# Kernel optimization log

Hardware: AMD Instinct MI355X
Metric: run time of the kernel (lower is better)

Reference implementation:

```python
import jax, jax.numpy as jnp
import numpy as np

HEADS = 16
LN_EPS = 1e-5


def setup_inputs() -> dict:
    key = jax.random.key(0)
    ks = jax.random.split(key, 12)
    B, IMG, Q, H = 8192, 2048, 768, 1024
    def init(k, shape, fan_in):
        return jax.random.normal(k, shape, dtype=jnp.float32) * (fan_in ** -0.5)
    return {
        "features1": jax.random.normal(ks[0], (B, IMG), dtype=jnp.float32),
        "features2": jax.random.normal(ks[1], (B, Q), dtype=jnp.float32),
        "W1": init(ks[2], (IMG, H), IMG),
        "b1": jnp.zeros((H,), dtype=jnp.float32),
        "W2": init(ks[3], (Q, H), Q),
        "b2": jnp.zeros((H,), dtype=jnp.float32),
        "Wqkv": init(ks[4], (H, 3 * H), H),
        "Wout": init(ks[5], (H, H), H),
        "bout": jnp.zeros((H,), dtype=jnp.float32),
        "gamma": jnp.ones((2 * H,), dtype=jnp.float32),
        "beta": jnp.zeros((2 * H,), dtype=jnp.float32),
    }


def reference(features1, features2, W1, b1, W2, b2, Wqkv, Wout, bout, gamma, beta):
    B = features1.shape[0]
    H = W1.shape[1]
    hd = H // HEADS
    scale = hd ** -0.5
    # modality projections -> [B, H] each
    f1 = features1 @ W1 + b1
    f2 = features2 @ W2 + b2
    x = jnp.stack([f1, f2], axis=1)                      # [B, 2, H]
    qkv = x @ Wqkv                                       # [B, 2, 3H]
    q, k, v = jnp.split(qkv, 3, axis=-1)
    # b n (h d) -> b h n d
    def to_heads(t):
        return t.reshape(B, 2, HEADS, hd).transpose(0, 2, 1, 3)
    q, k, v = to_heads(q) * scale, to_heads(k), to_heads(v)
    attn = jnp.einsum('bhid,bhjd->bhij', q, k)           # [B, h, 2, 2]
    attn = jax.nn.softmax(attn, axis=-1)
    out = jnp.einsum('bhij,bhjd->bhid', attn, v)         # [B, h, 2, d]
    out = out.transpose(0, 2, 1, 3).reshape(B, 2, H)     # b h n d -> b n (h d)
    out = out @ Wout + bout                              # [B, 2, H]
    flat = out.reshape(B, 2 * H)
    # LayerNorm over last dim
    mu = jnp.mean(flat, axis=-1, keepdims=True)
    var = jnp.var(flat, axis=-1, keepdims=True)
    normed = (flat - mu) * jax.lax.rsqrt(var + LN_EPS) * gamma + beta
    # dropout in eval mode = identity
    res = jnp.concatenate([f1, f2], axis=1)              # [B, 2H]
    return normed + res
```

## Files before the change

kernel.cpp:

```cpp
#include <hip/hip_runtime.h>
#include <hip/hip_bf16.h>
#include <cstdint>

typedef __attribute__((ext_vector_type(8))) short short8;
typedef __attribute__((ext_vector_type(4))) short short4v;
typedef __attribute__((ext_vector_type(4))) float floatx4;
typedef __attribute__((ext_vector_type(4))) unsigned short ushort4v;

__device__ __forceinline__ float bf2f(unsigned short u) {
    union { unsigned int u; float f; } v;
    v.u = ((unsigned int)u) << 16;
    return v.f;
}
__device__ __forceinline__ unsigned short f2bf(float f) {
    union { float f; unsigned int u; } v; v.f = f;
    unsigned int u = v.u;
    unsigned int r = (u + 0x7FFFu + ((u >> 16) & 1u)) >> 16;
    return (unsigned short)r;
}
__device__ __forceinline__ float lo_bf(unsigned int u) {
    union { unsigned int u; float f; } v; v.u = u << 16; return v.f;
}
__device__ __forceinline__ float hi_bf(unsigned int u) {
    union { unsigned int u; float f; } v; v.u = u & 0xffff0000u; return v.f;
}
__device__ __forceinline__ void gld_lds16(const void* g, void* l) {
    __builtin_amdgcn_global_load_lds(
        (const __attribute__((address_space(1))) unsigned int*)g,
        (__attribute__((address_space(3))) unsigned int*)l,
        16, 0, 0);
}

__global__ __launch_bounds__(256) void prep_kernel(
    const float* __restrict__ f1, const float* __restrict__ f2,
    unsigned short* __restrict__ f1b, unsigned short* __restrict__ f2b,
    const float* __restrict__ W1, unsigned short* __restrict__ W1t,
    const float* __restrict__ W2, unsigned short* __restrict__ W2t,
    const float* __restrict__ Wqkv, unsigned short* __restrict__ Wqkvt,
    const float* __restrict__ Wout, unsigned short* __restrict__ Woutt) {
    __shared__ float tile[64][33];
    const int b = blockIdx.x;
    const int tid = threadIdx.x;

    if (b < 5632) {
        const float* in = (b < 4096) ? f1 : f2;
        unsigned short* outp = (b < 4096) ? f1b : f2b;
        int base = ((b < 4096) ? b : (b - 4096)) * 1024 + tid;
#pragma unroll
        for (int it = 0; it < 4; it++) {
            int i = base + it * 256;
            float4 v = ((const float4*)in)[i];
            ushort4v o;
            o.x = f2bf(v.x); o.y = f2bf(v.y); o.z = f2bf(v.z); o.w = f2bf(v.w);
            ((ushort4v*)outp)[i] = o;
        }
        return;
    }

    const float* in; unsigned short* outp; int K, N, t;
    if (b < 6656)      { in = W1;   outp = W1t;   K = 2048; N = 1024; t = b - 5632; }
    else if (b < 7040) { in = W2;   outp = W2t;   K = 768;  N = 1024; t = b - 6656; }
    else if (b < 8576) { in = Wqkv; outp = Wqkvt; K = 1024; N = 3072; t = b - 7040; }
    else               { in = Wout; outp = Woutt; K = 1024; N = 1024; t = b - 8576; }
    const int ntiles = N >> 5;
    const int n0 = (t % ntiles) * 32;
    const int k0 = (t / ntiles) * 64;
    const int tx = tid & 31, tg = tid >> 5;
#pragma unroll
    for (int i = 0; i < 8; i++)
        tile[tg * 8 + i][tx] = in[(size_t)(k0 + tg * 8 + i) * N + n0 + tx];
    __syncthreads();
    const int n = tid >> 3, kc = (tid & 7) * 8;
    short8 o;
#pragma unroll
    for (int j = 0; j < 8; j++) o[j] = (short)f2bf(tile[kc + j][n]);
    *(short8*)&outp[(size_t)(n0 + n) * K + k0 + kc] = o;
}

template <bool OUT_BF16, bool HAS_BIAS>
__device__ __forceinline__ void gemm_core(const unsigned short* __restrict__ A,
                                          const unsigned short* __restrict__ Bt,
                                          void* __restrict__ Cv, const float* __restrict__ bias,
                                          int K, int ldc, int blockM, int blockN,
                                          unsigned short* As, unsigned short* Bs) {
    const int tid  = threadIdx.x;
    const int lane = tid & 63;
    const int wave = tid >> 6;
    const int wm = wave >> 1, wn = wave & 1;

    const int kx = (tid >> 3) & 3;
    const unsigned short* gA = A  + (size_t)(blockM + (tid >> 2)) * K + ((tid & 3) ^ kx) * 8;
    const unsigned short* gB = Bt + (size_t)(blockN + (tid >> 2)) * K + ((tid & 3) ^ kx) * 8;
    const size_t sK = (size_t)64 * K;
    unsigned short* lA = As + wave * 512;
    unsigned short* lB = Bs + wave * 512;

    floatx4 acc[4][4];
#pragma unroll
    for (int i = 0; i < 4; i++)
#pragma unroll
        for (int j = 0; j < 4; j++) acc[i][j] = (floatx4){0.f, 0.f, 0.f, 0.f};

    const int col  = lane & 15;
    const int quad = lane >> 4;
    const int qx = quad ^ ((col >> 1) & 3);
    const int aoff32 = (wm * 64 + col) * 32 + qx * 8;
    const int boff32 = (wn * 64 + col) * 32 + qx * 8;

    const int kIters = K >> 6;
    for (int kt = 0; kt < kIters; ++kt) {
        const size_t ko = (size_t)kt * 64;
        gld_lds16(gA + ko,           lA);
        gld_lds16(gA + sK + ko,      lA + 2048);
        gld_lds16(gA + 32 + ko,      lA + 4096);
        gld_lds16(gA + sK + 32 + ko, lA + 6144);
        gld_lds16(gB + ko,           lB);
        gld_lds16(gB + sK + ko,      lB + 2048);
        gld_lds16(gB + 32 + ko,      lB + 4096);
        gld_lds16(gB + sK + 32 + ko, lB + 6144);
        __syncthreads();

#pragma unroll
        for (int hh = 0; hh < 2; hh++) {
            short8 a[4];
#pragma unroll
            for (int i = 0; i < 4; i++) a[i] = *(const short8*)&As[hh * 4096 + aoff32 + i * 512];
#pragma unroll
            for (int j = 0; j < 4; j++) {
                short8 bj = *(const short8*)&Bs[hh * 4096 + boff32 + j * 512];
#pragma unroll
                for (int i = 0; i < 4; i++)
                    acc[i][j] = __builtin_amdgcn_mfma_f32_16x16x32_bf16(a[i], bj, acc[i][j], 0, 0, 0);
            }
        }
        __syncthreads();
    }

#pragma unroll
    for (int i = 0; i < 4; i++) {
#pragma unroll
        for (int j = 0; j < 4; j++) {
#pragma unroll
            for (int r = 0; r < 4; r++) {
                int row = blockM + wm * 64 + i * 16 + quad * 4 + r;
                int cn  = blockN + wn * 64 + j * 16 + col;
                float v = acc[i][j][r];
                if (HAS_BIAS) v += bias[cn];
                if (OUT_BF16) ((unsigned short*)Cv)[(size_t)row * ldc + cn] = f2bf(v);
                else          ((float*)Cv)[(size_t)row * ldc + cn] = v;
            }
        }
    }
}

__global__ __launch_bounds__(256, 3)
void gemm_f12(const unsigned short* __restrict__ f1b, const unsigned short* __restrict__ W1t,
              const float* __restrict__ b1,
              const unsigned short* __restrict__ f2b, const unsigned short* __restrict__ W2t,
              const float* __restrict__ b2, unsigned short* __restrict__ xb) {
    __shared__ alignas(16) unsigned short As[8192];
    __shared__ alignas(16) unsigned short Bs[8192];
    const int blockM = blockIdx.x * 128;
    const int blockN = blockIdx.y * 128;
    if (blockIdx.z == 0)
        gemm_core<true, true>(f1b, W1t, (void*)xb, b1, 2048, 2048, blockM, blockN, As, Bs);
    else
        gemm_core<true, true>(f2b, W2t, (void*)(xb + 1024), b2, 768, 2048, blockM, blockN, As, Bs);
}

__global__ __launch_bounds__(256, 3)
void gemm_proj(const unsigned short* __restrict__ attn, const unsigned short* __restrict__ Woutt,
               const float* __restrict__ bout, unsigned short* __restrict__ projb) {
    __shared__ alignas(16) unsigned short As[8192];
    __shared__ alignas(16) unsigned short Bs[8192];
    gemm_core<true, true>(attn, Woutt, (void*)projb, bout, 1024, 1024,
                          blockIdx.x * 128, blockIdx.y * 128, As, Bs);
}

#define T2_STRIDE 132
__global__ __launch_bounds__(256, 3)
void gemm_qkv_attn(const unsigned short* __restrict__ A, const unsigned short* __restrict__ Bt,
                   unsigned short* __restrict__ attn_out) {
    __shared__ alignas(16) char smem[52224];
    unsigned short* As = (unsigned short*)smem;
    unsigned short* Bs = As + 8192;
    unsigned short* T2 = (unsigned short*)smem;
    float* wsm = (float*)(smem + 50688);

    const int tid  = threadIdx.x;
    const int lane = tid & 63;
    const int wave = tid >> 6;
    const int g = blockIdx.x;
    const int h = g >> 7;
    const int blockM = (g & 127) * 128;
    const int wm = wave >> 1, wn = wave & 1;
    const int K = 1024;

    const int kx = (tid >> 3) & 3;
    const unsigned short* gA = A  + (size_t)(blockM + (tid >> 2)) * K + ((tid & 3) ^ kx) * 8;
    const unsigned short* gB = Bt + (size_t)(h * 64 + (tid >> 2)) * K + ((tid & 3) ^ kx) * 8;
    unsigned short* lA = As + wave * 512;
    unsigned short* lB = Bs + wave * 512;

    floatx4 acc[4][6];
#pragma unroll
    for (int i = 0; i < 4; i++)
#pragma unroll
        for (int j = 0; j < 6; j++) acc[i][j] = (floatx4){0.f, 0.f, 0.f, 0.f};

    const int col  = lane & 15;
    const int quad = lane >> 4;
    const int qx = quad ^ ((col >> 1) & 3);
    const int aoff32 = (wm * 64 + col) * 32 + qx * 8;
    const int boff32 = (wn * 96 + col) * 32 + qx * 8;

    for (int kt = 0; kt < 16; ++kt) {
        const size_t ko = (size_t)kt * 64;
        gld_lds16(gA + ko,               lA);
        gld_lds16(gA + 65536 + ko,       lA + 2048);
        gld_lds16(gA + 32 + ko,          lA + 4096);
        gld_lds16(gA + 65536 + 32 + ko,  lA + 6144);
        gld_lds16(gB + ko,               lB);
        gld_lds16(gB + 1048576 + ko,     lB + 2048);
        gld_lds16(gB + 2097152 + ko,     lB + 4096);
        gld_lds16(gB + 32 + ko,          lB + 6144);
        gld_lds16(gB + 1048576 + 32 + ko, lB + 8192);
        gld_lds16(gB + 2097152 + 32 + ko, lB + 10240);
        __syncthreads();

#pragma unroll
        for (int hh = 0; hh < 2; hh++) {
            short8 a[4];
#pragma unroll
            for (int i = 0; i < 4; i++) a[i] = *(const short8*)&As[hh * 4096 + aoff32 + i * 512];
#pragma unroll
            for (int j = 0; j < 6; j++) {
                short8 bj = *(const short8*)&Bs[hh * 6144 + boff32 + j * 512];
#pragma unroll
                for (int i = 0; i < 4; i++)
                    acc[i][j] = __builtin_amdgcn_mfma_f32_16x16x32_bf16(a[i], bj, acc[i][j], 0, 0, 0);
            }
        }
        __syncthreads();
    }

#pragma unroll
    for (int i = 0; i < 4; i++) {
#pragma unroll
        for (int j = 0; j < 6; j++) {
            int c  = wn * 96 + j * 16 + col;
            int r0 = wm * 64 + i * 16 + quad * 4;
            short4v pk;
            pk.x = (short)f2bf(acc[i][j][0]);
            pk.y = (short)f2bf(acc[i][j][1]);
            pk.z = (short)f2bf(acc[i][j][2]);
            pk.w = (short)f2bf(acc[i][j][3]);
            *(short4v*)&T2[c * T2_STRIDE + r0] = pk;
        }
    }
    __syncthreads();

    if (tid < 64) {
        const int ib = tid;
        float s00 = 0.f, s01 = 0.f, s10 = 0.f, s11 = 0.f;
#pragma unroll 8
        for (int d = 0; d < 64; d++) {
            unsigned int qp = *(const unsigned int*)&T2[d * T2_STRIDE + 2 * ib];
            unsigned int kp = *(const unsigned int*)&T2[(64 + d) * T2_STRIDE + 2 * ib];
            float q0 = lo_bf(qp), q1 = hi_bf(qp);
            float k0 = lo_bf(kp), k1 = hi_bf(kp);
            s00 += q0 * k0; s01 += q0 * k1;
            s10 += q1 * k0; s11 += q1 * k1;
        }
        const float sc = 0.125f;
        s00 *= sc; s01 *= sc; s10 *= sc; s11 *= sc;
        float m0 = fmaxf(s00, s01), m1 = fmaxf(s10, s11);
        float e00 = __expf(s00 - m0), e01 = __expf(s01 - m0);
        float e10 = __expf(s10 - m1), e11 = __expf(s11 - m1);
        float i0 = 1.f / (e00 + e01), i1 = 1.f / (e10 + e11);
        wsm[ib * 4 + 0] = e00 * i0; wsm[ib * 4 + 1] = e01 * i0;
        wsm[ib * 4 + 2] = e10 * i1; wsm[ib * 4 + 3] = e11 * i1;
    }
    __syncthreads();

#pragma unroll
    for (int gg = 0; gg < 4; gg++) {
        int chunk = gg * 256 + tid;
        int r = chunk >> 3;
        int dc = (chunk & 7) * 8;
        int ib = r >> 1, n = r & 1;
        float w0 = wsm[ib * 4 + n * 2 + 0];
        float w1 = wsm[ib * 4 + n * 2 + 1];
        short8 o;
#pragma unroll
        for (int dd = 0; dd < 8; dd++) {
            unsigned int vp = *(const unsigned int*)&T2[(128 + dc + dd) * T2_STRIDE + 2 * ib];
            o[dd] = (short)f2bf(w0 * lo_bf(vp) + w1 * hi_bf(vp));
        }
        *(short8*)&attn_out[(size_t)(blockM + r) * 1024 + h * 64 + dc] = o;
    }
}

__global__ __launch_bounds__(256) void ln_res_kernel(const unsigned short* __restrict__ proj,
                                                     const unsigned short* __restrict__ xres,
                                                     const float* __restrict__ gamma,
                                                     const float* __restrict__ beta,
                                                     float* __restrict__ out) {
    const int b = blockIdx.x;
    const int tid = threadIdx.x;
    const size_t base = (size_t)b * 2048;
    short8 p8 = ((const short8*)(proj + base))[tid];
    float pv[8];
#pragma unroll
    for (int e = 0; e < 8; e++) pv[e] = bf2f((unsigned short)p8[e]);
    float s = 0.f, ss = 0.f;
#pragma unroll
    for (int e = 0; e < 8; e++) { s += pv[e]; ss += pv[e] * pv[e]; }
#pragma unroll
    for (int off = 32; off > 0; off >>= 1) {
        s  += __shfl_xor(s, off);
        ss += __shfl_xor(ss, off);
    }
    __shared__ float red[8];
    const int wave = tid >> 6;
    if ((tid & 63) == 0) { red[wave] = s; red[4 + wave] = ss; }
    __syncthreads();
    s  = red[0] + red[1] + red[2] + red[3];
    ss = red[4] + red[5] + red[6] + red[7];
    const float mean = s * (1.0f / 2048.0f);
    const float var  = ss * (1.0f / 2048.0f) - mean * mean;
    const float rstd = rsqrtf(var + 1e-5f);

    const float4* g4 = (const float4*)gamma;
    const float4* b4 = (const float4*)beta;
    float4 g0 = g4[2 * tid], g1 = g4[2 * tid + 1];
    float4 be0 = b4[2 * tid], be1 = b4[2 * tid + 1];
    short8 r8 = ((const short8*)(xres + base))[tid];
    float4 o0, o1;
    o0.x = (pv[0] - mean) * rstd * g0.x + be0.x + bf2f((unsigned short)r8[0]);
    o0.y = (pv[1] - mean) * rstd * g0.y + be0.y + bf2f((unsigned short)r8[1]);
    o0.z = (pv[2] - mean) * rstd * g0.z + be0.z + bf2f((unsigned short)r8[2]);
    o0.w = (pv[3] - mean) * rstd * g0.w + be0.w + bf2f((unsigned short)r8[3]);
    o1.x = (pv[4] - mean) * rstd * g1.x + be1.x + bf2f((unsigned short)r8[4]);
    o1.y = (pv[5] - mean) * rstd * g1.y + be1.y + bf2f((unsigned short)r8[5]);
    o1.z = (pv[6] - mean) * rstd * g1.z + be1.z + bf2f((unsigned short)r8[6]);
    o1.w = (pv[7] - mean) * rstd * g1.w + be1.w + bf2f((unsigned short)r8[7]);
    float4* op = (float4*)(out + base);
    op[2 * tid] = o0;
    op[2 * tid + 1] = o1;
}

extern "C" void kernel_launch(void* const* d_in, const int* in_sizes, int n_in,
                              void* d_out, int out_size, void* d_ws, size_t ws_size,
                              hipStream_t stream) {
    (void)in_sizes; (void)n_in; (void)out_size; (void)ws_size;
    const float* features1 = (const float*)d_in[0];
    const float* features2 = (const float*)d_in[1];
    const float* W1   = (const float*)d_in[2];
    const float* b1   = (const float*)d_in[3];
    const float* W2   = (const float*)d_in[4];
    const float* b2   = (const float*)d_in[5];
    const float* Wqkv = (const float*)d_in[6];
    const float* Wout = (const float*)d_in[7];
    const float* bout = (const float*)d_in[8];
    const float* gamma = (const float*)d_in[9];
    const float* beta  = (const float*)d_in[10];
    float* out = (float*)d_out;

    char* ws = (char*)d_ws;
    unsigned short* f1b   = (unsigned short*)(ws);
    unsigned short* f2b   = (unsigned short*)(ws + 33554432);
    unsigned short* W1t   = (unsigned short*)(ws + 46137344);
    unsigned short* W2t   = (unsigned short*)(ws + 50331648);
    unsigned short* Wqkvt = (unsigned short*)(ws + 51904512);
    unsigned short* Woutt = (unsigned short*)(ws + 58195968);
    unsigned short* xb    = (unsigned short*)(ws + 60293120);
    unsigned short* attn  = (unsigned short*)(ws + 93847552);
    unsigned short* projb = (unsigned short*)(ws + 127401984);

    prep_kernel<<<9088, 256, 0, stream>>>(features1, features2, f1b, f2b,
                                          W1, W1t, W2, W2t, Wqkv, Wqkvt, Wout, Woutt);
    gemm_f12<<<dim3(64, 8, 2), 256, 0, stream>>>(f1b, W1t, b1, f2b, W2t, b2, xb);
    gemm_qkv_attn<<<2048, 256, 0, stream>>>(xb, Wqkvt, attn);
    gemm_proj<<<dim3(128, 8), 256, 0, stream>>>(attn, Woutt, bout, projb);
    ln_res_kernel<<<8192, 256, 0, stream>>>(projb, xb, gamma, beta, out);
}
```

Measured before the change: 373.1 us.

## Double-buffer fused QKV-attention GEMM with 256-row tiles and 512 threads

Rewrites the fused QKV+attention kernel so each block uses 512 threads over a 256-row M tile. It double-buffers LDS, prefetching the next K tile while MFMAs run, and uses a wider 64-element swizzled row layout. The K loop is split into four phases separated by explicit barriers and raised wave priority, to overlap global-to-LDS loads with compute and halve B-tile refetch per output row. The cost is about 114 KB of dynamic LDS per block, which limits occupancy, plus more barriers per iteration.

```diff
diff --git a/kernel.cpp b/kernel.cpp
--- a/kernel.cpp
+++ b/kernel.cpp
@@ -177,30 +177,42 @@
                           blockIdx.x * 128, blockIdx.y * 128, As, Bs);
 }
 
-#define T2_STRIDE 132
-__global__ __launch_bounds__(256, 3)
-void gemm_qkv_attn(const unsigned short* __restrict__ A, const unsigned short* __restrict__ Bt,
-                   unsigned short* __restrict__ attn_out) {
-    __shared__ alignas(16) char smem[52224];
-    unsigned short* As = (unsigned short*)smem;
-    unsigned short* Bs = As + 8192;
-    unsigned short* T2 = (unsigned short*)smem;
-    float* wsm = (float*)(smem + 50688);
+#define QKV_LDS_BYTES 116736
+#define T2_ST 264
+__global__ __launch_bounds__(512, 2)
+void gemm_qkv_attn2(const unsigned short* __restrict__ A, const unsigned short* __restrict__ Bt,
+                    unsigned short* __restrict__ attn_out) {
+    extern __shared__ __align__(16) char smem[];
+    unsigned short* buf0 = (unsigned short*)smem;
+    unsigned short* buf1 = (unsigned short*)(smem + 57344);
+    unsigned short* T2   = (unsigned short*)smem;
+    float* wsm = (float*)(smem + 114688);
 
     const int tid  = threadIdx.x;
     const int lane = tid & 63;
     const int wave = tid >> 6;
+    const int wm = wave >> 1;
+    const int wn = wave & 1;
     const int g = blockIdx.x;
-    const int h = g >> 7;
-    const int blockM = (g & 127) * 128;
-    const int wm = wave >> 1, wn = wave & 1;
+    const int h = g >> 6;
+    const int blockM = (g & 63) * 256;
     const int K = 1024;
 
-    const int kx = (tid >> 3) & 3;
-    const unsigned short* gA = A  + (size_t)(blockM + (tid >> 2)) * K + ((tid & 3) ^ kx) * 8;
-    const unsigned short* gB = Bt + (size_t)(h * 64 + (tid >> 2)) * K + ((tid & 3) ^ kx) * 8;
-    unsigned short* lA = As + wave * 512;
-    unsigned short* lB = Bs + wave * 512;
+    const int srow = tid >> 3;
+    const int schunk = (tid & 7) ^ (srow & 7);
+    const unsigned short* gA = A  + (size_t)(blockM + srow) * K + schunk * 8;
+    const unsigned short* gB = Bt + (size_t)(h * 64 + srow) * K + schunk * 8;
+    const int sdst = wave * 512;
+
+#define STAGE_A(bufp, koff) do { \
+    gld_lds16(gA + (koff),          (bufp) + sdst);          \
+    gld_lds16(gA + 65536 + (koff),  (bufp) + 4096 + sdst);   \
+    gld_lds16(gA + 131072 + (koff), (bufp) + 8192 + sdst);   \
+    gld_lds16(gA + 196608 + (koff), (bufp) + 12288 + sdst); } while (0)
+#define STAGE_B(bufp, koff) do { \
+    gld_lds16(gB + (koff),           (bufp) + 16384 + sdst);         \
+    gld_lds16(gB + 1048576 + (koff), (bufp) + 16384 + 4096 + sdst);  \
+    gld_lds16(gB + 2097152 + (koff), (bufp) + 16384 + 8192 + sdst); } while (0)
 
     floatx4 acc[4][6];
 #pragma unroll
@@ -210,39 +222,97 @@
 
     const int col  = lane & 15;
     const int quad = lane >> 4;
-    const int qx = quad ^ ((col >> 1) & 3);
-    const int aoff32 = (wm * 64 + col) * 32 + qx * 8;
-    const int boff32 = (wn * 96 + col) * 32 + qx * 8;
+    const int ch0  = (quad ^ (col & 7)) * 8;
+    int aoff[4], boff[6];
+#pragma unroll
+    for (int i = 0; i < 4; i++) aoff[i] = (wm * 64 + i * 16 + col) * 64 + ch0;
+#pragma unroll
+    for (int j = 0; j < 6; j++) boff[j] = 16384 + (wn * 96 + j * 16 + col) * 64 + ch0;
+
+    STAGE_A(buf0, 0);
+    STAGE_B(buf0, 0);
 
     for (int kt = 0; kt < 16; ++kt) {
-        const size_t ko = (size_t)kt * 64;
-        gld_lds16(gA + ko,               lA);
-        gld_lds16(gA + 65536 + ko,       lA + 2048);
-        gld_lds16(gA + 32 + ko,          lA + 4096);
-        gld_lds16(gA + 65536 + 32 + ko,  lA + 6144);
-        gld_lds16(gB + ko,               lB);
-        gld_lds16(gB + 1048576 + ko,     lB + 2048);
-        gld_lds16(gB + 2097152 + ko,     lB + 4096);
-        gld_lds16(gB + 32 + ko,          lB + 6144);
-        gld_lds16(gB + 1048576 + 32 + ko, lB + 8192);
-        gld_lds16(gB + 2097152 + 32 + ko, lB + 10240);
+        unsigned short* cur = (kt & 1) ? buf1 : buf0;
+        unsigned short* nxt = (kt & 1) ? buf0 : buf1;
+        const int kn = (kt + 1) * 64;
         __syncthreads();
 
-#pragma unroll
-        for (int hh = 0; hh < 2; hh++) {
-            short8 a[4];
-#pragma unroll
-            for (int i = 0; i < 4; i++) a[i] = *(const short8*)&As[hh * 4096 + aoff32 + i * 512];
-#pragma unroll
-            for (int j = 0; j < 6; j++) {
-                short8 bj = *(const short8*)&Bs[hh * 6144 + boff32 + j * 512];
-#pragma unroll
-                for (int i = 0; i < 4; i++)
-                    acc[i][j] = __builtin_amdgcn_mfma_f32_16x16x32_bf16(a[i], bj, acc[i][j], 0, 0, 0);
-            }
-        }
-        __syncthreads();
-    }
+        short8 a0[4], b0v[3];
+#pragma unroll
+        for (int i = 0; i < 4; i++) a0[i] = *(const short8*)&cur[aoff[i]];
+#pragma unroll
+        for (int j = 0; j < 3; j++) b0v[j] = *(const short8*)&cur[boff[j]];
+        if (kt < 15) { STAGE_A(nxt, kn); }
+        __builtin_amdgcn_sched_barrier(0);
+        __builtin_amdgcn_s_barrier();
+        asm volatile("s_waitcnt lgkmcnt(0)" ::: "memory");
+        __builtin_amdgcn_sched_barrier(0);
+        __builtin_amdgcn_s_setprio(1);
+#pragma unroll
+        for (int j = 0; j < 3; j++)
+#pragma unroll
+            for (int i = 0; i < 4; i++)
+                acc[i][j] = __builtin_amdgcn_mfma_f32_16x16x32_bf16(a0[i], b0v[j], acc[i][j], 0, 0, 0);
+        __builtin_amdgcn_s_setprio(0);
+        __builtin_amdgcn_sched_barrier(0);
+        __builtin_amdgcn_s_barrier();
+
+        short8 b1v[3];
+#pragma unroll
+        for (int j = 0; j < 3; j++) b1v[j] = *(const short8*)&cur[boff[3 + j]];
+        if (kt < 15) { STAGE_B(nxt, kn); }
+        __builtin_amdgcn_sched_barrier(0);
+        __builtin_amdgcn_s_barrier();
+        asm volatile("s_waitcnt lgkmcnt(0)" ::: "memory");
+        __builtin_amdgcn_sched_barrier(0);
+        __builtin_amdgcn_s_setprio(1);
+#pragma unroll
+        for (int j = 0; j < 3; j++)
+#pragma unroll
+            for (int i = 0; i < 4; i++)
+                acc[i][3 + j] = __builtin_amdgcn_mfma_f32_16x16x32_bf16(a0[i], b1v[j], acc[i][3 + j], 0, 0, 0);
+        __builtin_amdgcn_s_setprio(0);
+        __builtin_amdgcn_sched_barrier(0);
+        __builtin_amdgcn_s_barrier();
+
+        short8 a1[4], b2v[3];
+#pragma unroll
+        for (int i = 0; i < 4; i++) a1[i] = *(const short8*)&cur[aoff[i] ^ 32];
+#pragma unroll
+        for (int j = 0; j < 3; j++) b2v[j] = *(const short8*)&cur[boff[j] ^ 32];
+        __builtin_amdgcn_sched_barrier(0);
+        __builtin_amdgcn_s_barrier();
+        asm volatile("s_waitcnt lgkmcnt(0)" ::: "memory");
+        __builtin_amdgcn_sched_barrier(0);
+        __builtin_amdgcn_s_setprio(1);
+#pragma unroll
+        for (int j = 0; j < 3; j++)
+#pragma unroll
+            for (int i = 0; i < 4; i++)
+                acc[i][j] = __builtin_amdgcn_mfma_f32_16x16x32_bf16(a1[i], b2v[j], acc[i][j], 0, 0, 0);
+        __builtin_amdgcn_s_setprio(0);
+        __builtin_amdgcn_sched_barrier(0);
+        __builtin_amdgcn_s_barrier();
+
+        short8 b3v[3];
+#pragma unroll
+        for (int j = 0; j < 3; j++) b3v[j] = *(const short8*)&cur[boff[3 + j] ^ 32];
+        __builtin_amdgcn_sched_barrier(0);
+        __builtin_amdgcn_s_barrier();
+        asm volatile("s_waitcnt lgkmcnt(0)" ::: "memory");
+        __builtin_amdgcn_sched_barrier(0);
+        __builtin_amdgcn_s_setprio(1);
+#pragma unroll
+        for (int j = 0; j < 3; j++)
+#pragma unroll
+            for (int i = 0; i < 4; i++)
+                acc[i][3 + j] = __builtin_amdgcn_mfma_f32_16x16x32_bf16(a1[i], b3v[j], acc[i][3 + j], 0, 0, 0);
+        __builtin_amdgcn_s_setprio(0);
+    }
+    __syncthreads();
+#undef STAGE_A
+#undef STAGE_B
 
 #pragma unroll
     for (int i = 0; i < 4; i++) {
@@ -255,18 +325,18 @@
             pk.y = (short)f2bf(acc[i][j][1]);
             pk.z = (short)f2bf(acc[i][j][2]);
             pk.w = (short)f2bf(acc[i][j][3]);
-            *(short4v*)&T2[c * T2_STRIDE + r0] = pk;
+            *(short4v*)&T2[c * T2_ST + r0] = pk;
         }
     }
     __syncthreads();
 
-    if (tid < 64) {
+    if (tid < 128) {
         const int ib = tid;
         float s00 = 0.f, s01 = 0.f, s10 = 0.f, s11 = 0.f;
 #pragma unroll 8
         for (int d = 0; d < 64; d++) {
-            unsigned int qp = *(const unsigned int*)&T2[d * T2_STRIDE + 2 * ib];
-            unsigned int kp = *(const unsigned int*)&T2[(64 + d) * T2_STRIDE + 2 * ib];
+            unsigned int qp = *(const unsigned int*)&T2[d * T2_ST + 2 * ib];
+            unsigned int kp = *(const unsigned int*)&T2[(64 + d) * T2_ST + 2 * ib];
             float q0 = lo_bf(qp), q1 = hi_bf(qp);
             float k0 = lo_bf(kp), k1 = hi_bf(kp);
             s00 += q0 * k0; s01 += q0 * k1;
@@ -285,7 +355,7 @@
 
 #pragma unroll
     for (int gg = 0; gg < 4; gg++) {
-        int chunk = gg * 256 + tid;
+        int chunk = gg * 512 + tid;
         int r = chunk >> 3;
         int dc = (chunk & 7) * 8;
         int ib = r >> 1, n = r & 1;
@@ -294,7 +364,7 @@
         short8 o;
 #pragma unroll
         for (int dd = 0; dd < 8; dd++) {
-            unsigned int vp = *(const unsigned int*)&T2[(128 + dc + dd) * T2_STRIDE + 2 * ib];
+            unsigned int vp = *(const unsigned int*)&T2[(128 + dc + dd) * T2_ST + 2 * ib];
             o[dd] = (short)f2bf(w0 * lo_bf(vp) + w1 * hi_bf(vp));
         }
         *(short8*)&attn_out[(size_t)(blockM + r) * 1024 + h * 64 + dc] = o;
@@ -367,6 +437,14 @@
     const float* beta  = (const float*)d_in[10];
     float* out = (float*)d_out;
 
+    static bool qkv2_init = false;
+    if (!qkv2_init) {
+        (void)hipFuncSetAttribute((const void*)gemm_qkv_attn2,
+                                  hipFuncAttributeMaxDynamicSharedMemorySize,
+                                  QKV_LDS_BYTES);
+        qkv2_init = true;
+    }
+
     char* ws = (char*)d_ws;
     unsigned short* f1b   = (unsigned short*)(ws);
     unsigned short* f2b   = (unsigned short*)(ws + 33554432);
@@ -381,7 +459,7 @@
     prep_kernel<<<9088, 256, 0, stream>>>(features1, features2, f1b, f2b,
                                           W1, W1t, W2, W2t, Wqkv, Wqkvt, Wout, Woutt);
     gemm_f12<<<dim3(64, 8, 2), 256, 0, stream>>>(f1b, W1t, b1, f2b, W2t, b2, xb);
-    gemm_qkv_attn<<<2048, 256, 0, stream>>>(xb, Wqkvt, attn);
+    gemm_qkv_attn2<<<1024, 512, QKV_LDS_BYTES, stream>>>(xb, Wqkvt, attn);
     gemm_proj<<<dim3(128, 8), 256, 0, stream>>>(attn, Woutt, bout, projb);
     ln_res_kernel<<<8192, 256, 0, stream>>>(projb, xb, gamma, beta, out);
 }
```

Result: slower. 389.1 us (+4.3%).

## Double-buffer LDS in fused QKV-attention GEMM to overlap loads with MFMA

Applied to the files above, without the earlier changes.

Replaces the single-buffered K loop in the fused QKV+attention kernel with a two-stage LDS ping-pong, prefetching the next K tile while computing on the current one. It uses explicit vmcnt/lgkmcnt waits, sched barriers and s_setprio around the MFMA blocks. Dynamic shared memory grows to 80 KB and launch bounds drop from 3 to 2 blocks per CU, trading occupancy for latency hiding. The barrier placement is hand-tuned and carries a risk of races between the prefetch and the reads of the other buffer.

```diff
diff --git a/kernel.cpp b/kernel.cpp
--- a/kernel.cpp
+++ b/kernel.cpp
@@ -177,15 +177,16 @@
                           blockIdx.x * 128, blockIdx.y * 128, As, Bs);
 }
 
-#define T2_STRIDE 132
-__global__ __launch_bounds__(256, 3)
-void gemm_qkv_attn(const unsigned short* __restrict__ A, const unsigned short* __restrict__ Bt,
-                   unsigned short* __restrict__ attn_out) {
-    __shared__ alignas(16) char smem[52224];
-    unsigned short* As = (unsigned short*)smem;
-    unsigned short* Bs = As + 8192;
-    unsigned short* T2 = (unsigned short*)smem;
-    float* wsm = (float*)(smem + 50688);
+#define QKV_LDS_BYTES 81920
+#define T2_ST 132
+__global__ __launch_bounds__(256, 2)
+void gemm_qkv_attn3(const unsigned short* __restrict__ A, const unsigned short* __restrict__ Bt,
+                    unsigned short* __restrict__ attn_out) {
+    extern __shared__ __align__(16) char smem[];
+    unsigned short* buf0 = (unsigned short*)smem;
+    unsigned short* buf1 = buf0 + 20480;
+    unsigned short* T2   = (unsigned short*)smem;
+    float* wsm = (float*)(smem + 51200);
 
     const int tid  = threadIdx.x;
     const int lane = tid & 63;
@@ -199,8 +200,20 @@
     const int kx = (tid >> 3) & 3;
     const unsigned short* gA = A  + (size_t)(blockM + (tid >> 2)) * K + ((tid & 3) ^ kx) * 8;
     const unsigned short* gB = Bt + (size_t)(h * 64 + (tid >> 2)) * K + ((tid & 3) ^ kx) * 8;
-    unsigned short* lA = As + wave * 512;
-    unsigned short* lB = Bs + wave * 512;
+
+#define STAGE(p, ko) do {                                                   \
+    unsigned short* lA = (p) + wave * 512;                                  \
+    unsigned short* lB = (p) + 8192 + wave * 512;                           \
+    gld_lds16(gA + (ko),                lA);            \
+    gld_lds16(gA + 65536 + (ko),        lA + 2048);    \
+    gld_lds16(gA + 32 + (ko),           lA + 4096);     \
+    gld_lds16(gA + 65536 + 32 + (ko),   lA + 6144);    \
+    gld_lds16(gB + (ko),                lB);                       \
+    gld_lds16(gB + 1048576 + (ko),      lB + 2048);                \
+    gld_lds16(gB + 2097152 + (ko),      lB + 4096);                \
+    gld_lds16(gB + 32 + (ko),           lB + 6144);                \
+    gld_lds16(gB + 1048576 + 32 + (ko), lB + 8192);                \
+    gld_lds16(gB + 2097152 + 32 + (ko), lB + 10240);    } while (0)
 
     floatx4 acc[4][6];
 #pragma unroll
@@ -212,37 +225,54 @@
     const int quad = lane >> 4;
     const int qx = quad ^ ((col >> 1) & 3);
     const int aoff32 = (wm * 64 + col) * 32 + qx * 8;
-    const int boff32 = (wn * 96 + col) * 32 + qx * 8;
+    const int boff32 = 8192 + (wn * 96 + col) * 32 + qx * 8;
+
+    STAGE(buf0, 0);
 
     for (int kt = 0; kt < 16; ++kt) {
-        const size_t ko = (size_t)kt * 64;
-        gld_lds16(gA + ko,               lA);
-        gld_lds16(gA + 65536 + ko,       lA + 2048);
-        gld_lds16(gA + 32 + ko,          lA + 4096);
-        gld_lds16(gA + 65536 + 32 + ko,  lA + 6144);
-        gld_lds16(gB + ko,               lB);
-        gld_lds16(gB + 1048576 + ko,     lB + 2048);
-        gld_lds16(gB + 2097152 + ko,     lB + 4096);
-        gld_lds16(gB + 32 + ko,          lB + 6144);
-        gld_lds16(gB + 1048576 + 32 + ko, lB + 8192);
-        gld_lds16(gB + 2097152 + 32 + ko, lB + 10240);
-        __syncthreads();
-
-#pragma unroll
-        for (int hh = 0; hh < 2; hh++) {
-            short8 a[4];
-#pragma unroll
-            for (int i = 0; i < 4; i++) a[i] = *(const short8*)&As[hh * 4096 + aoff32 + i * 512];
-#pragma unroll
-            for (int j = 0; j < 6; j++) {
-                short8 bj = *(const short8*)&Bs[hh * 6144 + boff32 + j * 512];
-#pragma unroll
-                for (int i = 0; i < 4; i++)
-                    acc[i][j] = __builtin_amdgcn_mfma_f32_16x16x32_bf16(a[i], bj, acc[i][j], 0, 0, 0);
-            }
-        }
-        __syncthreads();
-    }
+        unsigned short* cur = (kt & 1) ? buf1 : buf0;
+        unsigned short* nxt = (kt & 1) ? buf0 : buf1;
+        if (kt < 15) {
+            STAGE(nxt, (size_t)(kt + 1) * 64);
+            asm volatile("s_waitcnt vmcnt(10)" ::: "memory");
+        } else {
+            asm volatile("s_waitcnt vmcnt(0)" ::: "memory");
+        }
+        __builtin_amdgcn_sched_barrier(0);
+        __builtin_amdgcn_s_barrier();
+
+        short8 a0[4], b0v[6];
+#pragma unroll
+        for (int i = 0; i < 4; i++) a0[i] = *(const short8*)&cur[aoff32 + i * 512];
+#pragma unroll
+        for (int j = 0; j < 6; j++) b0v[j] = *(const short8*)&cur[boff32 + j * 512];
+        asm volatile("s_waitcnt lgkmcnt(0)" ::: "memory");
+        __builtin_amdgcn_sched_barrier(0);
+        __builtin_amdgcn_s_setprio(1);
+#pragma unroll
+        for (int j = 0; j < 6; j++)
+#pragma unroll
+            for (int i = 0; i < 4; i++)
+                acc[i][j] = __builtin_amdgcn_mfma_f32_16x16x32_bf16(a0[i], b0v[j], acc[i][j], 0, 0, 0);
+        __builtin_amdgcn_s_setprio(0);
+
+        short8 a1[4], b1v[6];
+#pragma unroll
+        for (int i = 0; i < 4; i++) a1[i] = *(const short8*)&cur[4096 + aoff32 + i * 512];
+#pragma unroll
+        for (int j = 0; j < 6; j++) b1v[j] = *(const short8*)&cur[6144 + boff32 + j * 512];
+        asm volatile("s_waitcnt lgkmcnt(0)" ::: "memory");
+        __builtin_amdgcn_sched_barrier(0);
+        __builtin_amdgcn_s_barrier();
+        __builtin_amdgcn_s_setprio(1);
+#pragma unroll
+        for (int j = 0; j < 6; j++)
+#pragma unroll
+            for (int i = 0; i < 4; i++)
+                acc[i][j] = __builtin_amdgcn_mfma_f32_16x16x32_bf16(a1[i], b1v[j], acc[i][j], 0, 0, 0);
+        __builtin_amdgcn_s_setprio(0);
+    }
+#undef STAGE
 
 #pragma unroll
     for (int i = 0; i < 4; i++) {
@@ -255,7 +285,7 @@
             pk.y = (short)f2bf(acc[i][j][1]);
             pk.z = (short)f2bf(acc[i][j][2]);
             pk.w = (short)f2bf(acc[i][j][3]);
-            *(short4v*)&T2[c * T2_STRIDE + r0] = pk;
+            *(short4v*)&T2[c * T2_ST + r0] = pk;
         }
     }
     __syncthreads();
@@ -265,8 +295,8 @@
         float s00 = 0.f, s01 = 0.f, s10 = 0.f, s11 = 0.f;
 #pragma unroll 8
         for (int d = 0; d < 64; d++) {
-            unsigned int qp = *(const unsigned int*)&T2[d * T2_STRIDE + 2 * ib];
-            unsigned int kp = *(const unsigned int*)&T2[(64 + d) * T2_STRIDE + 2 * ib];
+            unsigned int qp = *(const unsigned int*)&T2[d * T2_ST + 2 * ib];
+            unsigned int kp = *(const unsigned int*)&T2[(64 + d) * T2_ST + 2 * ib];
             float q0 = lo_bf(qp), q1 = hi_bf(qp);
             float k0 = lo_bf(kp), k1 = hi_bf(kp);
             s00 += q0 * k0; s01 += q0 * k1;
@@ -294,7 +324,7 @@
         short8 o;
 #pragma unroll
         for (int dd = 0; dd < 8; dd++) {
-            unsigned int vp = *(const unsigned int*)&T2[(128 + dc + dd) * T2_STRIDE + 2 * ib];
+            unsigned int vp = *(const unsigned int*)&T2[(128 + dc + dd) * T2_ST + 2 * ib];
             o[dd] = (short)f2bf(w0 * lo_bf(vp) + w1 * hi_bf(vp));
         }
         *(short8*)&attn_out[(size_t)(blockM + r) * 1024 + h * 64 + dc] = o;
@@ -367,6 +397,14 @@
     const float* beta  = (const float*)d_in[10];
     float* out = (float*)d_out;
 
+    static bool qkv3_init = false;
+    if (!qkv3_init) {
+        (void)hipFuncSetAttribute((const void*)gemm_qkv_attn3,
+                                  hipFuncAttributeMaxDynamicSharedMemorySize,
+                                  QKV_LDS_BYTES);
+        qkv3_init = true;
+    }
+
     char* ws = (char*)d_ws;
     unsigned short* f1b   = (unsigned short*)(ws);
     unsigned short* f2b   = (unsigned short*)(ws + 33554432);
@@ -381,7 +419,7 @@
     prep_kernel<<<9088, 256, 0, stream>>>(features1, features2, f1b, f2b,
                                           W1, W1t, W2, W2t, Wqkv, Wqkvt, Wout, Woutt);
     gemm_f12<<<dim3(64, 8, 2), 256, 0, stream>>>(f1b, W1t, b1, f2b, W2t, b2, xb);
-    gemm_qkv_attn<<<2048, 256, 0, stream>>>(xb, Wqkvt, attn);
+    gemm_qkv_attn3<<<2048, 256, QKV_LDS_BYTES, stream>>>(xb, Wqkvt, attn);
     gemm_proj<<<dim3(128, 8), 256, 0, stream>>>(attn, Woutt, bout, projb);
     ln_res_kernel<<<8192, 256, 0, stream>>>(projb, xb, gamma, beta, out);
 }
```

Result: no change. 370.4 us (-0.7%).

## Double-buffer LDS with async prefetch in both GEMM main loops

Applied to the files above, without the earlier changes.

Both GEMM cores now split K into 32-wide half tiles held in two LDS buffers. The global-to-LDS loads for stage s+2 are issued while stage s runs its MFMAs, and the per-iteration pair of __syncthreads is replaced by explicit vmcnt/lgkmcnt waits and raw s_barrier calls. MFMA sections are also raised with s_setprio. This is meant to hide global memory latency behind compute, at the cost of more barriers per K step and fragile hand-counted waitcnt values.

```diff
diff --git a/kernel.cpp b/kernel.cpp
--- a/kernel.cpp
+++ b/kernel.cpp
@@ -92,8 +92,7 @@
     const unsigned short* gA = A  + (size_t)(blockM + (tid >> 2)) * K + ((tid & 3) ^ kx) * 8;
     const unsigned short* gB = Bt + (size_t)(blockN + (tid >> 2)) * K + ((tid & 3) ^ kx) * 8;
     const size_t sK = (size_t)64 * K;
-    unsigned short* lA = As + wave * 512;
-    unsigned short* lB = Bs + wave * 512;
+    const int wo = wave * 512;
 
     floatx4 acc[4][4];
 #pragma unroll
@@ -107,34 +106,45 @@
     const int aoff32 = (wm * 64 + col) * 32 + qx * 8;
     const int boff32 = (wn * 64 + col) * 32 + qx * 8;
 
-    const int kIters = K >> 6;
-    for (int kt = 0; kt < kIters; ++kt) {
-        const size_t ko = (size_t)kt * 64;
-        gld_lds16(gA + ko,           lA);
-        gld_lds16(gA + sK + ko,      lA + 2048);
-        gld_lds16(gA + 32 + ko,      lA + 4096);
-        gld_lds16(gA + sK + 32 + ko, lA + 6144);
-        gld_lds16(gB + ko,           lB);
-        gld_lds16(gB + sK + ko,      lB + 2048);
-        gld_lds16(gB + 32 + ko,      lB + 4096);
-        gld_lds16(gB + sK + 32 + ko, lB + 6144);
-        __syncthreads();
-
-#pragma unroll
-        for (int hh = 0; hh < 2; hh++) {
-            short8 a[4];
-#pragma unroll
-            for (int i = 0; i < 4; i++) a[i] = *(const short8*)&As[hh * 4096 + aoff32 + i * 512];
-#pragma unroll
-            for (int j = 0; j < 4; j++) {
-                short8 bj = *(const short8*)&Bs[hh * 4096 + boff32 + j * 512];
-#pragma unroll
-                for (int i = 0; i < 4; i++)
-                    acc[i][j] = __builtin_amdgcn_mfma_f32_16x16x32_bf16(a[i], bj, acc[i][j], 0, 0, 0);
-            }
-        }
-        __syncthreads();
-    }
+    const int nhalf = K >> 5;
+
+#define CSTAGE(s, REG) do {                                               \
+    const size_t kof = (size_t)(s) * 32;                                  \
+    gld_lds16(gA + kof,      As + (REG) * 4096 + wo);                     \
+    gld_lds16(gA + sK + kof, As + (REG) * 4096 + 2048 + wo);              \
+    gld_lds16(gB + kof,      Bs + (REG) * 4096 + wo);                     \
+    gld_lds16(gB + sK + kof, Bs + (REG) * 4096 + 2048 + wo); } while (0)
+
+#define CHALF(s, REG) do {                                                \
+    if ((s) < nhalf - 1) asm volatile("s_waitcnt vmcnt(4)" ::: "memory"); \
+    else                 asm volatile("s_waitcnt vmcnt(0)" ::: "memory"); \
+    __builtin_amdgcn_sched_barrier(0);                                    \
+    __builtin_amdgcn_s_barrier();              \
+    short8 a[4], bv[4];                                                   \
+    _Pragma("unroll")                                                     \
+    for (int i = 0; i < 4; i++) a[i]  = *(const short8*)&As[(REG) * 4096 + aoff32 + i * 512]; \
+    _Pragma("unroll")                                                     \
+    for (int j = 0; j < 4; j++) bv[j] = *(const short8*)&Bs[(REG) * 4096 + boff32 + j * 512]; \
+    asm volatile("s_waitcnt lgkmcnt(0)" ::: "memory");                    \
+    __builtin_amdgcn_sched_barrier(0);                                    \
+    __builtin_amdgcn_s_barrier();         \
+    if ((s) + 2 < nhalf) CSTAGE((s) + 2, REG);                            \
+    __builtin_amdgcn_s_setprio(1);                                        \
+    _Pragma("unroll")                                                     \
+    for (int j = 0; j < 4; j++)                                           \
+        _Pragma("unroll")                                                 \
+        for (int i = 0; i < 4; i++)                                       \
+            acc[i][j] = __builtin_amdgcn_mfma_f32_16x16x32_bf16(a[i], bv[j], acc[i][j], 0, 0, 0); \
+    __builtin_amdgcn_s_setprio(0); } while (0)
+
+    CSTAGE(0, 0);
+    CSTAGE(1, 1);
+    for (int st = 0; st < nhalf; st += 2) {
+        CHALF(st, 0);
+        CHALF(st + 1, 1);
+    }
+#undef CSTAGE
+#undef CHALF
 
 #pragma unroll
     for (int i = 0; i < 4; i++) {
@@ -199,8 +209,7 @@
     const int kx = (tid >> 3) & 3;
     const unsigned short* gA = A  + (size_t)(blockM + (tid >> 2)) * K + ((tid & 3) ^ kx) * 8;
     const unsigned short* gB = Bt + (size_t)(h * 64 + (tid >> 2)) * K + ((tid & 3) ^ kx) * 8;
-    unsigned short* lA = As + wave * 512;
-    unsigned short* lB = Bs + wave * 512;
+    const int wo = wave * 512;
 
     floatx4 acc[4][6];
 #pragma unroll
@@ -214,35 +223,49 @@
     const int aoff32 = (wm * 64 + col) * 32 + qx * 8;
     const int boff32 = (wn * 96 + col) * 32 + qx * 8;
 
-    for (int kt = 0; kt < 16; ++kt) {
-        const size_t ko = (size_t)kt * 64;
-        gld_lds16(gA + ko,               lA);
-        gld_lds16(gA + 65536 + ko,       lA + 2048);
-        gld_lds16(gA + 32 + ko,          lA + 4096);
-        gld_lds16(gA + 65536 + 32 + ko,  lA + 6144);
-        gld_lds16(gB + ko,               lB);
-        gld_lds16(gB + 1048576 + ko,     lB + 2048);
-        gld_lds16(gB + 2097152 + ko,     lB + 4096);
-        gld_lds16(gB + 32 + ko,          lB + 6144);
-        gld_lds16(gB + 1048576 + 32 + ko, lB + 8192);
-        gld_lds16(gB + 2097152 + 32 + ko, lB + 10240);
-        __syncthreads();
-
-#pragma unroll
-        for (int hh = 0; hh < 2; hh++) {
-            short8 a[4];
-#pragma unroll
-            for (int i = 0; i < 4; i++) a[i] = *(const short8*)&As[hh * 4096 + aoff32 + i * 512];
-#pragma unroll
-            for (int j = 0; j < 6; j++) {
-                short8 bj = *(const short8*)&Bs[hh * 6144 + boff32 + j * 512];
-#pragma unroll
-                for (int i = 0; i < 4; i++)
-                    acc[i][j] = __builtin_amdgcn_mfma_f32_16x16x32_bf16(a[i], bj, acc[i][j], 0, 0, 0);
-            }
-        }
-        __syncthreads();
-    }
+    const int nhalf = 32;
+
+#define QSTAGE(s, REG) do {                                               \
+    const size_t kof = (size_t)(s) * 32;                                  \
+    gld_lds16(gA + kof,           As + (REG) * 4096 + wo);                \
+    gld_lds16(gA + 65536 + kof,   As + (REG) * 4096 + 2048 + wo);         \
+    gld_lds16(gB + kof,           Bs + (REG) * 6144 + wo);           \
+    gld_lds16(gB + 1048576 + kof, Bs + (REG) * 6144 + 2048 + wo);    \
+    gld_lds16(gB + 2097152 + kof, Bs + (REG) * 6144 + 4096 + wo);    \
+    } while (0)
+
+#define QHALF(s, REG) do {                                                \
+    if ((s) < nhalf - 1) asm volatile("s_waitcnt vmcnt(5)" ::: "memory"); \
+    else                 asm volatile("s_waitcnt vmcnt(0)" ::: "memory"); \
+    __builtin_amdgcn_sched_barrier(0);                                    \
+    __builtin_amdgcn_s_barrier();              \
+    short8 a[4], bv[6];                                                   \
+    _Pragma("unroll")                                                     \
+    for (int i = 0; i < 4; i++) a[i]  = *(const short8*)&As[(REG) * 4096 + aoff32 + i * 512]; \
+    _Pragma("unroll")                                                     \
+    for (int j = 0; j < 6; j++) bv[j] = *(const short8*)&Bs[(REG) * 6144 + boff32 + j * 512]; \
+    asm volatile("s_waitcnt lgkmcnt(0)" ::: "memory");                    \
+    __builtin_amdgcn_sched_barrier(0);                                    \
+    __builtin_amdgcn_s_barrier();         \
+    if ((s) + 2 < nhalf) QSTAGE((s) + 2, REG);                            \
+    __builtin_amdgcn_s_setprio(1);                                        \
+    _Pragma("unroll")                                                     \
+    for (int j = 0; j < 6; j++)                                           \
+        _Pragma("unroll")                                                 \
+        for (int i = 0; i < 4; i++)                                       \
+            acc[i][j] = __builtin_amdgcn_mfma_f32_16x16x32_bf16(a[i], bv[j], acc[i][j], 0, 0, 0); \
+    __builtin_amdgcn_s_setprio(0); } while (0)
+
+    QSTAGE(0, 0);
+    QSTAGE(1, 1);
+    for (int st = 0; st < nhalf; st += 2) {
+        QHALF(st, 0);
+        QHALF(st + 1, 1);
+    }
+#undef QSTAGE
+#undef QHALF
+
+    __syncthreads();
 
 #pragma unroll
     for (int i = 0; i < 4; i++) {
```

After: 401.6 us. +7.6%, slower.
